# Kernel tuning notes

Measured on AMD Instinct MI355X. Metric: run time of the kernel, lower is better.

The kernel has to match this reference:

```python
import jax, jax.numpy as jnp
import numpy as np

B, T, H = 8, 2048, 1024
THRESHOLD = 0.9
MAX_HOP = 12
LN_EPS = 1e-5


def setup_inputs() -> dict:
    key = jax.random.key(0)
    ks = jax.random.split(key, 5)
    inputs = jax.random.normal(ks[0], (B, T, H), jnp.float32)
    time_enc = jax.random.normal(ks[1], (1, T, H), jnp.float32)
    pos_enc = jax.random.normal(ks[2], (1, MAX_HOP, H), jnp.float32)
    ln_gamma = jnp.ones((H,), jnp.float32)
    ln_beta = jnp.zeros((H,), jnp.float32)
    w_p = jax.random.normal(ks[3], (H,), jnp.float32) / np.float32(np.sqrt(H))
    b_p = jnp.ones((1,), jnp.float32)  # p.bias.data.fill_(1)
    Wt = jax.random.normal(ks[4], (H, H), jnp.float32) / np.float32(np.sqrt(H))
    bt = jnp.zeros((H,), jnp.float32)
    return dict(inputs=inputs, time_enc=time_enc, pos_enc=pos_enc,
                ln_gamma=ln_gamma, ln_beta=ln_beta, w_p=w_p, b_p=b_p,
                Wt=Wt, bt=bt)


def _act_forward(inputs, time_enc, pos_enc, ln_gamma, ln_beta, w_p, b_p, Wt, bt):
    Bv, Tv, _ = inputs.shape
    base = inputs + time_enc[:, :Tv]  # [B,T,H]

    def step(carry, k):
        hp, rem, n_up, prev = carry
        state = base + pos_enc[:, k][:, None, :]  # [B,T,H]
        # LayerNorm
        mu = state.mean(-1, keepdims=True)
        var = state.var(-1, keepdims=True)
        normed = (state - mu) * jax.lax.rsqrt(var + LN_EPS) * ln_gamma + ln_beta
        # halting probability [B,T]
        p = jax.nn.sigmoid(jnp.einsum('bth,h->bt', normed, w_p) + b_p[0])
        sr = (hp < 1.0).astype(state.dtype)
        acc = hp + p * sr
        nh = (acc > THRESHOLD).astype(state.dtype) * sr
        sr = (acc <= THRESHOLD).astype(state.dtype) * sr
        hp = hp + p * sr
        rem = rem + nh * (1.0 - hp)
        hp = hp + nh * rem
        n_up = n_up + sr + nh
        # state update (transformation_fn modeled as Linear Wt, bt)
        uw = (p * sr + nh * rem)[..., None]  # [B,T,1]
        tstate = jnp.einsum('bth,oh->bto', state, Wt) + bt
        new = tstate * uw + prev * (1.0 - uw)
        return (hp, rem, n_up, new), None

    z = jnp.zeros((Bv, Tv), inputs.dtype)
    init = (z, z, z, jnp.zeros_like(inputs))
    # Fixed MAX_HOP iterations: once all tokens halt, still_running and
    # new_halted are identically zero so further steps are exact no-ops,
    # matching the data-dependent while loop of the original module.
    (hp, rem, n_up, prev), _ = jax.lax.scan(step, init, jnp.arange(MAX_HOP))
    return prev, rem, n_up


def reference(inputs, time_enc, pos_enc, ln_gamma, ln_beta, w_p, b_p, Wt, bt):
    return _act_forward(inputs, time_enc, pos_enc, ln_gamma, ln_beta, w_p, b_p, Wt, bt)
```

## Files before the change

kernel.cpp:

```cpp
#include <hip/hip_runtime.h>


#define Hdim 1024
#define Ntok 16384
#define Tdim 2048
#define KHOP 12

typedef unsigned short u16;
typedef __attribute__((ext_vector_type(8))) short bf16x8;
typedef __attribute__((ext_vector_type(4))) float floatx4;
struct __align__(8) u16x4 { u16 x, y, z, w; };

static __device__ inline u16 f2bf(float f) {
    union { float f; unsigned u; } x; x.f = f;
    unsigned r = x.u + 0x7FFFu + ((x.u >> 16) & 1u);
    return (u16)(r >> 16);
}

__global__ __launch_bounds__(256)
void ptwt_kernel(const float* __restrict__ pos,
                 const float* __restrict__ gamma,
                 const float* __restrict__ beta,
                 const float* __restrict__ wp,
                 const float* __restrict__ Wt,
                 float* __restrict__ kst,
                 float* __restrict__ gwArr,
                 float* __restrict__ PT,
                 u16* __restrict__ WtBF) {
    if (blockIdx.x < 13) {
        int lane = threadIdx.x;
        if (lane >= 64) return;
        int b = blockIdx.x;
        if (b == 12) {
            float gw = 0.f, bw = 0.f;
#pragma unroll
            for (int i = 0; i < 16; i++) {
                int h = lane + 64 * i;
                float g = gamma[h] * wp[h];
                gwArr[h] = g;
                gw += g;
                bw += beta[h] * wp[h];
            }
            for (int off = 32; off > 0; off >>= 1) {
                gw += __shfl_xor(gw, off);
                bw += __shfl_xor(bw, off);
            }
            if (lane == 0) { kst[36] = gw; kst[37] = bw; }
        } else {
            int k = b;
            float gw = 0.f;
#pragma unroll
            for (int i = 0; i < 16; i++) {
                int h = lane + 64 * i;
                gw += gamma[h] * wp[h];
            }
            for (int off = 32; off > 0; off >>= 1) gw += __shfl_xor(gw, off);
            float s = 0.f, ss = 0.f, pg = 0.f;
#pragma unroll
            for (int i = 0; i < 16; i++) {
                int h = lane + 64 * i;
                float v = pos[k * Hdim + h];
                s += v; ss += v * v; pg += v * gamma[h] * wp[h];
            }
            for (int off = 32; off > 0; off >>= 1) {
                s += __shfl_xor(s, off);
                ss += __shfl_xor(ss, off);
                pg += __shfl_xor(pg, off);
            }
            if (lane == 0) {
                float mu = s * (1.0f / Hdim);
                kst[k] = mu;
                kst[12 + k] = ss - (float)Hdim * mu * mu;
                kst[24 + k] = pg - mu * gw;
            }
        }
        return;
    }

    __shared__ float red[4][KHOP];
    int o = blockIdx.x - 13;
    int t = threadIdx.x, wave = t >> 6, lane = t & 63;

    float4 w = ((const float4*)(Wt + (size_t)o * Hdim))[t];
    u16x4 ob; ob.x = f2bf(w.x); ob.y = f2bf(w.y); ob.z = f2bf(w.z); ob.w = f2bf(w.w);
    ((u16x4*)(WtBF + (size_t)o * Hdim))[t] = ob;

    const float4* pos4 = (const float4*)pos;
    float acc[KHOP];
#pragma unroll
    for (int k = 0; k < KHOP; k++) {
        float4 p = pos4[k * 256 + t];
        acc[k] = w.x * p.x + w.y * p.y + w.z * p.z + w.w * p.w;
    }
#pragma unroll
    for (int k = 0; k < KHOP; k++)
        for (int off = 32; off > 0; off >>= 1) acc[k] += __shfl_xor(acc[k], off);
    if (lane == 0) {
#pragma unroll
        for (int k = 0; k < KHOP; k++) red[wave][k] = acc[k];
    }
    __syncthreads();
    if (t < KHOP)
        PT[t * Hdim + o] = red[0][t] + red[1][t] + red[2][t] + red[3][t];
}

__global__ __launch_bounds__(512)
void token_kernel(const float* __restrict__ inp, const float* __restrict__ tenc,
                  const float* __restrict__ pos, const float* __restrict__ gwArr,
                  const float* __restrict__ bp, const float* __restrict__ kst,
                  float* __restrict__ SS, float* __restrict__ WW,
                  float* __restrict__ tail, u16* __restrict__ baseBF) {
    __shared__ float sPos[KHOP * Hdim];
    int t = threadIdx.x;
    for (int i = t; i < KHOP * Hdim; i += 512) sPos[i] = pos[i];
    __syncthreads();

    int wave = t >> 6, lane = t & 63;
    int grp = lane >> 4, s = lane & 15;
    int n = blockIdx.x * 32 + wave * 4 + grp;

    const float4* ip4 = (const float4*)(inp + (size_t)n * Hdim);
    const float4* tp4 = (const float4*)(tenc + (size_t)(n & (Tdim - 1)) * Hdim);
    u16x4* ob4 = (u16x4*)(baseBF + (size_t)n * Hdim);
    const float4* gw4 = (const float4*)gwArr;

    float sm = 0.f, ss = 0.f, d1 = 0.f;
    float dk[KHOP];
#pragma unroll
    for (int k = 0; k < KHOP; k++) dk[k] = 0.f;

#pragma unroll
    for (int i = 0; i < 16; i++) {
        int idx = s + 16 * i;
        float4 a = ip4[idx], b = tp4[idx];
        float4 v = make_float4(a.x + b.x, a.y + b.y, a.z + b.z, a.w + b.w);
        u16x4 o; o.x = f2bf(v.x); o.y = f2bf(v.y); o.z = f2bf(v.z); o.w = f2bf(v.w);
        ob4[idx] = o;
        sm += v.x + v.y + v.z + v.w;
        ss += v.x * v.x + v.y * v.y + v.z * v.z + v.w * v.w;
        float4 g = gw4[idx];
        d1 += v.x * g.x + v.y * g.y + v.z * g.z + v.w * g.w;
        int h = idx * 4;
#pragma unroll
        for (int k = 0; k < KHOP; k++) {
            float4 p = *(const float4*)&sPos[k * Hdim + h];
            dk[k] += v.x * p.x + v.y * p.y + v.z * p.z + v.w * p.w;
        }
    }
#pragma unroll
    for (int off = 8; off > 0; off >>= 1) {
        sm += __shfl_xor(sm, off);
        ss += __shfl_xor(ss, off);
        d1 += __shfl_xor(d1, off);
#pragma unroll
        for (int k = 0; k < KHOP; k++) dk[k] += __shfl_xor(dk[k], off);
    }

    if (s == 0) {
        float gwv = kst[36], bwv = kst[37], bpv = bp[0];
        float mu = sm * (1.0f / Hdim);
        float ssb = ss - (float)Hdim * mu * mu;
        float hp = 0.f, rem = 0.f, nu = 0.f;
        float uw[KHOP];
#pragma unroll
        for (int k = 0; k < KHOP; k++) {
            float mup = kst[k], sspk = kst[12 + k], ek = kst[24 + k];
            float ck = dk[k] - (float)Hdim * mu * mup;
            float var = (ssb + sspk + 2.0f * ck) * (1.0f / Hdim);
            float inv = 1.0f / sqrtf(var + 1e-5f);
            float logit = inv * (d1 - mu * gwv + ek) + bwv + bpv;
            float p = 1.0f / (1.0f + expf(-logit));
            float sr = (hp < 1.0f) ? 1.0f : 0.0f;
            float acc = hp + p * sr;
            float nh = (acc > 0.9f) ? sr : 0.0f;
            float sr2 = (acc <= 0.9f) ? sr : 0.0f;
            hp += p * sr2;
            rem += nh * (1.0f - hp);
            hp += nh * rem;
            nu += sr2 + nh;
            uw[k] = p * sr2 + nh * rem;
        }
        float prod = 1.f, S = 0.f;
        float w[KHOP];
#pragma unroll
        for (int k = KHOP - 1; k >= 0; k--) {
            w[k] = uw[k] * prod;
            prod *= (1.0f - uw[k]);
            S += w[k];
        }
        SS[n] = S;
#pragma unroll
        for (int k = 0; k < KHOP; k++) WW[k * Ntok + n] = w[k];
        tail[n] = rem;
        tail[Ntok + n] = nu;
    }
}

__global__ __launch_bounds__(512, 2)
void gemm_bf16(const u16* __restrict__ A, const u16* __restrict__ Bt,
               const float* __restrict__ bt, const float* __restrict__ PT,
               const float* __restrict__ SS, const float* __restrict__ WW,
               float* __restrict__ out) {
    extern __shared__ u16 lds[];
    const int tid = threadIdx.x;
    const int bm = blockIdx.x;
    const int bn = blockIdx.y;
    const int gm = bm * 256, gn = bn * 256;

    const int sr = tid >> 3;
    const int gchunk = ((tid & 7) ^ (sr & 7)) << 3;
    const u16* aStage = A + (size_t)(gm + sr) * Hdim + gchunk;
    const u16* bStage = Bt + (size_t)(gn + sr) * Hdim + gchunk;
    char* ldsA = (char*)lds + (size_t)tid * 16;
    char* ldsB = (char*)lds + 65536 + (size_t)tid * 16;

#define STAGE_TILE(kt_)                                                          \
    do {                                                                         \
        const int s_ = (kt_) & 1;                                                \
        const u16* ap_ = aStage + (kt_) * 64;                                    \
        const u16* bp_ = bStage + (kt_) * 64;                                    \
        char* la_ = ldsA + s_ * 32768;                                           \
        char* lb_ = ldsB + s_ * 32768;                                           \
        _Pragma("unroll")                                                        \
        for (int i_ = 0; i_ < 4; i_++) {                                         \
            __builtin_amdgcn_global_load_lds(                                    \
                (const __attribute__((address_space(1))) void*)(ap_ + (size_t)i_ * 64 * Hdim), \
                (__attribute__((address_space(3))) void*)(la_ + i_ * 8192), 16, 0, 0); \
            __builtin_amdgcn_global_load_lds(                                    \
                (const __attribute__((address_space(1))) void*)(bp_ + (size_t)i_ * 64 * Hdim), \
                (__attribute__((address_space(3))) void*)(lb_ + i_ * 8192), 16, 0, 0); \
        }                                                                        \
    } while (0)

    STAGE_TILE(0);
    STAGE_TILE(1);

    const int wave = tid >> 6, lane = tid & 63;
    const int wr = wave >> 2, wc = wave & 3;
    const int quad = lane >> 4, l16 = lane & 15;
    const int xorl = l16 & 7;
    const int pos0 = ((quad ^ xorl) << 3);
    const int pos1 = (((4 + quad) ^ xorl) << 3);
    const u16* aRd = lds + (size_t)(128 * wr + l16) * 64;
    const u16* bRd = lds + 32768 + (size_t)(64 * wc + l16) * 64;

    floatx4 acc[8][4];
#pragma unroll
    for (int i = 0; i < 8; i++)
#pragma unroll
        for (int j = 0; j < 4; j++) acc[i][j] = (floatx4)0.f;

#pragma unroll 2
    for (int kt = 0; kt < 16; kt++) {
        const int s = kt & 1;
        if (kt < 15) { asm volatile("s_waitcnt vmcnt(8)" ::: "memory"); }
        else         { asm volatile("s_waitcnt vmcnt(0)" ::: "memory"); }
        asm volatile("s_barrier" ::: "memory");

        const u16* aS = aRd + s * 16384;
        const u16* bS = bRd + s * 16384;
        bf16x8 a[4][2], b[4][2];
#pragma unroll
        for (int ni = 0; ni < 4; ni++) {
            b[ni][0] = *(const bf16x8*)&bS[ni * 1024 + pos0];
            b[ni][1] = *(const bf16x8*)&bS[ni * 1024 + pos1];
        }
#pragma unroll
        for (int mi = 0; mi < 4; mi++) {
            a[mi][0] = *(const bf16x8*)&aS[mi * 1024 + pos0];
            a[mi][1] = *(const bf16x8*)&aS[mi * 1024 + pos1];
        }
        __builtin_amdgcn_s_setprio(1);
#pragma unroll
        for (int kk = 0; kk < 2; kk++)
#pragma unroll
            for (int mi = 0; mi < 4; mi++)
#pragma unroll
                for (int ni = 0; ni < 4; ni++)
                    acc[mi][ni] = __builtin_amdgcn_mfma_f32_16x16x32_bf16(
                        a[mi][kk], b[ni][kk], acc[mi][ni], 0, 0, 0);
        __builtin_amdgcn_s_setprio(0);

#pragma unroll
        for (int mi = 0; mi < 4; mi++) {
            a[mi][0] = *(const bf16x8*)&aS[4096 + mi * 1024 + pos0];
            a[mi][1] = *(const bf16x8*)&aS[4096 + mi * 1024 + pos1];
        }
        asm volatile("s_barrier" ::: "memory");
        if (kt < 14) STAGE_TILE(kt + 2);
        __builtin_amdgcn_s_setprio(1);
#pragma unroll
        for (int kk = 0; kk < 2; kk++)
#pragma unroll
            for (int mi = 0; mi < 4; mi++)
#pragma unroll
                for (int ni = 0; ni < 4; ni++)
                    acc[4 + mi][ni] = __builtin_amdgcn_mfma_f32_16x16x32_bf16(
                        a[mi][kk], b[ni][kk], acc[4 + mi][ni], 0, 0, 0);
        __builtin_amdgcn_s_setprio(0);
    }
#undef STAGE_TILE

    const int colBase = gn + 64 * wc;
    float btc[4], PTc[KHOP][4];
#pragma unroll
    for (int ni = 0; ni < 4; ni++) {
        int col = colBase + 16 * ni + l16;
        btc[ni] = bt[col];
#pragma unroll
        for (int k = 0; k < KHOP; k++) PTc[k][ni] = PT[k * Hdim + col];
    }
    const int rowBase = gm + 128 * wr;
#pragma unroll
    for (int mi = 0; mi < 8; mi++) {
        int r0 = rowBase + 16 * mi + quad * 4;
        float Sr[4], Wr[KHOP][4];
#pragma unroll
        for (int reg = 0; reg < 4; reg++) Sr[reg] = SS[r0 + reg];
#pragma unroll
        for (int k = 0; k < KHOP; k++)
#pragma unroll
            for (int reg = 0; reg < 4; reg++) Wr[k][reg] = WW[k * Ntok + r0 + reg];
#pragma unroll
        for (int ni = 0; ni < 4; ni++) {
            int col = colBase + 16 * ni + l16;
#pragma unroll
            for (int reg = 0; reg < 4; reg++) {
                float v = Sr[reg] * (acc[mi][ni][reg] + btc[ni]);
#pragma unroll
                for (int k = 0; k < KHOP; k++) v += Wr[k][reg] * PTc[k][ni];
                out[(size_t)(r0 + reg) * Hdim + col] = v;
            }
        }
    }
}

extern "C" void kernel_launch(void* const* d_in, const int* in_sizes, int n_in,
                              void* d_out, int out_size, void* d_ws, size_t ws_size,
                              hipStream_t stream) {
    const float* inp   = (const float*)d_in[0];
    const float* tenc  = (const float*)d_in[1];
    const float* pos   = (const float*)d_in[2];
    const float* gamma = (const float*)d_in[3];
    const float* beta  = (const float*)d_in[4];
    const float* wp    = (const float*)d_in[5];
    const float* bp    = (const float*)d_in[6];
    const float* Wt    = (const float*)d_in[7];
    const float* bt    = (const float*)d_in[8];
    float* out = (float*)d_out;

    float* W = (float*)d_ws;
    float* kst = W;
    float* gwArr = W + 64;
    float* PT  = gwArr + Hdim;
    float* SS  = PT + KHOP * Hdim;
    float* WW  = SS + Ntok;
    u16* WtBF  = (u16*)(WW + KHOP * Ntok);
    u16* baseBF = WtBF + (size_t)Hdim * Hdim;

    static bool attr_done = false;
    if (!attr_done) {
        (void)hipFuncSetAttribute((const void*)gemm_bf16,
                                  hipFuncAttributeMaxDynamicSharedMemorySize,
                                  131072);
        attr_done = true;
    }

    ptwt_kernel<<<1037, 256, 0, stream>>>(pos, gamma, beta, wp, Wt,
                                          kst, gwArr, PT, WtBF);
    token_kernel<<<512, 512, 0, stream>>>(inp, tenc, pos, gwArr, bp, kst,
                                          SS, WW, out + (size_t)Ntok * Hdim, baseBF);
    gemm_bf16<<<dim3(64, 4), 512, 131072, stream>>>(baseBF, WtBF, bt, PT, SS, WW, out);
}
```

Baseline: 193.2 us.

## Deepen GEMM pipeline to 4-stage BK=32 ring and prefetch token loads

The bf16 GEMM's K loop changes from 16 double-buffered BK=64 tiles with two barriers per step to 32 BK=32 tiles in a four-slot LDS ring, keeping three tiles in flight with a single barrier per step and a new XOR swizzle. The token kernel now software-prefetches its input and time-encoding loads two iterations ahead and declares an occupancy hint of 4 blocks per CU. The aim is to hide global-load latency better and cut barrier count, at the cost of smaller MFMA batches per barrier and possible register pressure in the token kernel.

```diff
diff --git a/kernel.cpp b/kernel.cpp
--- a/kernel.cpp
+++ b/kernel.cpp
@@ -104,7 +104,7 @@
         PT[t * Hdim + o] = red[0][t] + red[1][t] + red[2][t] + red[3][t];
 }
 
-__global__ __launch_bounds__(512)
+__global__ __launch_bounds__(512, 4)
 void token_kernel(const float* __restrict__ inp, const float* __restrict__ tenc,
                   const float* __restrict__ pos, const float* __restrict__ gwArr,
                   const float* __restrict__ bp, const float* __restrict__ kst,
@@ -129,10 +129,15 @@
 #pragma unroll
     for (int k = 0; k < KHOP; k++) dk[k] = 0.f;
 
+    float4 pa0 = ip4[s],      pb0 = tp4[s];
+    float4 pa1 = ip4[s + 16], pb1 = tp4[s + 16];
+
 #pragma unroll
     for (int i = 0; i < 16; i++) {
         int idx = s + 16 * i;
-        float4 a = ip4[idx], b = tp4[idx];
+        float4 a = pa0, b = pb0;
+        pa0 = pa1; pb0 = pb1;
+        if (i < 14) { pa1 = ip4[idx + 32]; pb1 = tp4[idx + 32]; }
         float4 v = make_float4(a.x + b.x, a.y + b.y, a.z + b.z, a.w + b.w);
         u16x4 o; o.x = f2bf(v.x); o.y = f2bf(v.y); o.z = f2bf(v.z); o.w = f2bf(v.w);
         ob4[idx] = o;
@@ -207,42 +212,37 @@
     const int bn = blockIdx.y;
     const int gm = bm * 256, gn = bn * 256;
 
-    const int sr = tid >> 3;
-    const int gchunk = ((tid & 7) ^ (sr & 7)) << 3;
-    const u16* aStage = A + (size_t)(gm + sr) * Hdim + gchunk;
-    const u16* bStage = Bt + (size_t)(gn + sr) * Hdim + gchunk;
-    char* ldsA = (char*)lds + (size_t)tid * 16;
-    char* ldsB = (char*)lds + 65536 + (size_t)tid * 16;
+    const int gch = (((tid & 3) ^ ((tid >> 3) & 3)) << 3);
+    const u16* aStage = A + (size_t)(gm + (tid >> 2)) * Hdim + gch;
+    const u16* bStage = Bt + (size_t)(gn + (tid >> 2)) * Hdim + gch;
+    char* ldsW = (char*)lds + (size_t)tid * 16;
+
+#define GLDS(src_, dstoff_)                                                      \
+    __builtin_amdgcn_global_load_lds(                                            \
+        (const __attribute__((address_space(1))) void*)(src_),                   \
+        (__attribute__((address_space(3))) void*)(ldsW + (dstoff_)), 16, 0, 0)
 
 #define STAGE_TILE(kt_)                                                          \
     do {                                                                         \
-        const int s_ = (kt_) & 1;                                                \
-        const u16* ap_ = aStage + (kt_) * 64;                                    \
-        const u16* bp_ = bStage + (kt_) * 64;                                    \
-        char* la_ = ldsA + s_ * 32768;                                           \
-        char* lb_ = ldsB + s_ * 32768;                                           \
-        _Pragma("unroll")                                                        \
-        for (int i_ = 0; i_ < 4; i_++) {                                         \
-            __builtin_amdgcn_global_load_lds(                                    \
-                (const __attribute__((address_space(1))) void*)(ap_ + (size_t)i_ * 64 * Hdim), \
-                (__attribute__((address_space(3))) void*)(la_ + i_ * 8192), 16, 0, 0); \
-            __builtin_amdgcn_global_load_lds(                                    \
-                (const __attribute__((address_space(1))) void*)(bp_ + (size_t)i_ * 64 * Hdim), \
-                (__attribute__((address_space(3))) void*)(lb_ + i_ * 8192), 16, 0, 0); \
-        }                                                                        \
+        const int so_ = ((kt_) & 3) * 32768;                                     \
+        const u16* ap_ = aStage + (kt_) * 32;                                    \
+        const u16* bp_ = bStage + (kt_) * 32;                                    \
+        GLDS(ap_,                 so_);                     \
+        GLDS(ap_ + 128 * Hdim,    so_ + 8192);              \
+        GLDS(bp_,                 so_ + 16384);             \
+        GLDS(bp_ + 128 * Hdim,    so_ + 24576);             \
     } while (0)
 
     STAGE_TILE(0);
     STAGE_TILE(1);
+    STAGE_TILE(2);
 
     const int wave = tid >> 6, lane = tid & 63;
     const int wr = wave >> 2, wc = wave & 3;
     const int quad = lane >> 4, l16 = lane & 15;
-    const int xorl = l16 & 7;
-    const int pos0 = ((quad ^ xorl) << 3);
-    const int pos1 = (((4 + quad) ^ xorl) << 3);
-    const u16* aRd = lds + (size_t)(128 * wr + l16) * 64;
-    const u16* bRd = lds + 32768 + (size_t)(64 * wc + l16) * 64;
+    const int pos = ((quad ^ ((l16 >> 1) & 3)) << 3);
+    const u16* aRd = lds + (size_t)(128 * wr + l16) * 32 + pos;
+    const u16* bRd = lds + 8192 + (size_t)(64 * wc + l16) * 32 + pos;
 
     floatx4 acc[8][4];
 #pragma unroll
@@ -250,56 +250,35 @@
 #pragma unroll
         for (int j = 0; j < 4; j++) acc[i][j] = (floatx4)0.f;
 
-#pragma unroll 2
-    for (int kt = 0; kt < 16; kt++) {
-        const int s = kt & 1;
-        if (kt < 15) { asm volatile("s_waitcnt vmcnt(8)" ::: "memory"); }
-        else         { asm volatile("s_waitcnt vmcnt(0)" ::: "memory"); }
+#pragma unroll 4
+    for (int kt = 0; kt < 32; kt++) {
+        if (kt <= 29)      { asm volatile("s_waitcnt vmcnt(8)" ::: "memory"); }
+        else if (kt == 30) { asm volatile("s_waitcnt vmcnt(4)" ::: "memory"); }
+        else               { asm volatile("s_waitcnt vmcnt(0)" ::: "memory"); }
         asm volatile("s_barrier" ::: "memory");
 
-        const u16* aS = aRd + s * 16384;
-        const u16* bS = bRd + s * 16384;
-        bf16x8 a[4][2], b[4][2];
-#pragma unroll
-        for (int ni = 0; ni < 4; ni++) {
-            b[ni][0] = *(const bf16x8*)&bS[ni * 1024 + pos0];
-            b[ni][1] = *(const bf16x8*)&bS[ni * 1024 + pos1];
-        }
-#pragma unroll
-        for (int mi = 0; mi < 4; mi++) {
-            a[mi][0] = *(const bf16x8*)&aS[mi * 1024 + pos0];
-            a[mi][1] = *(const bf16x8*)&aS[mi * 1024 + pos1];
-        }
+        if (kt <= 28) STAGE_TILE(kt + 3);
+
+        const int so = (kt & 3) * 16384;
+        const u16* aS = aRd + so;
+        const u16* bS = bRd + so;
+        bf16x8 a[8], b[4];
+#pragma unroll
+        for (int ni = 0; ni < 4; ni++) b[ni] = *(const bf16x8*)&bS[ni * 512];
+#pragma unroll
+        for (int mi = 0; mi < 8; mi++) a[mi] = *(const bf16x8*)&aS[mi * 512];
+
         __builtin_amdgcn_s_setprio(1);
 #pragma unroll
-        for (int kk = 0; kk < 2; kk++)
-#pragma unroll
-            for (int mi = 0; mi < 4; mi++)
-#pragma unroll
-                for (int ni = 0; ni < 4; ni++)
-                    acc[mi][ni] = __builtin_amdgcn_mfma_f32_16x16x32_bf16(
-                        a[mi][kk], b[ni][kk], acc[mi][ni], 0, 0, 0);
+        for (int mi = 0; mi < 8; mi++)
+#pragma unroll
+            for (int ni = 0; ni < 4; ni++)
+                acc[mi][ni] = __builtin_amdgcn_mfma_f32_16x16x32_bf16(
+                    a[mi], b[ni], acc[mi][ni], 0, 0, 0);
         __builtin_amdgcn_s_setprio(0);
-
-#pragma unroll
-        for (int mi = 0; mi < 4; mi++) {
-            a[mi][0] = *(const bf16x8*)&aS[4096 + mi * 1024 + pos0];
-            a[mi][1] = *(const bf16x8*)&aS[4096 + mi * 1024 + pos1];
-        }
-        asm volatile("s_barrier" ::: "memory");
-        if (kt < 14) STAGE_TILE(kt + 2);
-        __builtin_amdgcn_s_setprio(1);
-#pragma unroll
-        for (int kk = 0; kk < 2; kk++)
-#pragma unroll
-            for (int mi = 0; mi < 4; mi++)
-#pragma unroll
-                for (int ni = 0; ni < 4; ni++)
-                    acc[4 + mi][ni] = __builtin_amdgcn_mfma_f32_16x16x32_bf16(
-                        a[mi][kk], b[ni][kk], acc[4 + mi][ni], 0, 0, 0);
-        __builtin_amdgcn_s_setprio(0);
     }
 #undef STAGE_TILE
+#undef GLDS
 
     const int colBase = gn + 64 * wc;
     float btc[4], PTc[KHOP][4];
```

Result: slower. 223.6 us (+15.8%).

## Use 4-wave GEMM blocks with 128x128 warp tiles and prefetch token loads

Applied to the files above, without the earlier changes.

The GEMM block drops from 8 waves to 4, and each wave now computes a 128x128 sub-tile (8x8 MFMA accumulators) instead of 128x64. This raises register-level reuse of the A and B fragments and halves LDS reads per MFMA. Staging is redistributed so each thread issues twice as many global-to-LDS loads, and the wait counts are adjusted to match. The token kernel also gets software-prefetched input loads and an occupancy hint. The larger accumulator array (256 floats per lane) risks high VGPR pressure or spills, and fewer waves per CU means less latency hiding.

```diff
diff --git a/kernel.cpp b/kernel.cpp
--- a/kernel.cpp
+++ b/kernel.cpp
@@ -104,7 +104,7 @@
         PT[t * Hdim + o] = red[0][t] + red[1][t] + red[2][t] + red[3][t];
 }
 
-__global__ __launch_bounds__(512)
+__global__ __launch_bounds__(512, 4)
 void token_kernel(const float* __restrict__ inp, const float* __restrict__ tenc,
                   const float* __restrict__ pos, const float* __restrict__ gwArr,
                   const float* __restrict__ bp, const float* __restrict__ kst,
@@ -129,10 +129,15 @@
 #pragma unroll
     for (int k = 0; k < KHOP; k++) dk[k] = 0.f;
 
+    float4 pa0 = ip4[s],      pb0 = tp4[s];
+    float4 pa1 = ip4[s + 16], pb1 = tp4[s + 16];
+
 #pragma unroll
     for (int i = 0; i < 16; i++) {
         int idx = s + 16 * i;
-        float4 a = ip4[idx], b = tp4[idx];
+        float4 a = pa0, b = pb0;
+        pa0 = pa1; pb0 = pb1;
+        if (i < 14) { pa1 = ip4[idx + 32]; pb1 = tp4[idx + 32]; }
         float4 v = make_float4(a.x + b.x, a.y + b.y, a.z + b.z, a.w + b.w);
         u16x4 o; o.x = f2bf(v.x); o.y = f2bf(v.y); o.z = f2bf(v.z); o.w = f2bf(v.w);
         ob4[idx] = o;
@@ -196,7 +201,7 @@
     }
 }
 
-__global__ __launch_bounds__(512, 2)
+__global__ __launch_bounds__(256, 1)
 void gemm_bf16(const u16* __restrict__ A, const u16* __restrict__ Bt,
                const float* __restrict__ bt, const float* __restrict__ PT,
                const float* __restrict__ SS, const float* __restrict__ WW,
@@ -214,6 +219,11 @@
     char* ldsA = (char*)lds + (size_t)tid * 16;
     char* ldsB = (char*)lds + 65536 + (size_t)tid * 16;
 
+#define GLDS(src_, dst_)                                                         \
+    __builtin_amdgcn_global_load_lds(                                            \
+        (const __attribute__((address_space(1))) void*)(src_),                   \
+        (__attribute__((address_space(3))) void*)(dst_), 16, 0, 0)
+
 #define STAGE_TILE(kt_)                                                          \
     do {                                                                         \
         const int s_ = (kt_) & 1;                                                \
@@ -222,13 +232,9 @@
         char* la_ = ldsA + s_ * 32768;                                           \
         char* lb_ = ldsB + s_ * 32768;                                           \
         _Pragma("unroll")                                                        \
-        for (int i_ = 0; i_ < 4; i_++) {                                         \
-            __builtin_amdgcn_global_load_lds(                                    \
-                (const __attribute__((address_space(1))) void*)(ap_ + (size_t)i_ * 64 * Hdim), \
-                (__attribute__((address_space(3))) void*)(la_ + i_ * 8192), 16, 0, 0); \
-            __builtin_amdgcn_global_load_lds(                                    \
-                (const __attribute__((address_space(1))) void*)(bp_ + (size_t)i_ * 64 * Hdim), \
-                (__attribute__((address_space(3))) void*)(lb_ + i_ * 8192), 16, 0, 0); \
+        for (int i_ = 0; i_ < 8; i_++) {                                         \
+            GLDS(ap_ + (size_t)i_ * 32 * Hdim, la_ + i_ * 4096);                 \
+            GLDS(bp_ + (size_t)i_ * 32 * Hdim, lb_ + i_ * 4096);                 \
         }                                                                        \
     } while (0)
 
@@ -236,75 +242,64 @@
     STAGE_TILE(1);
 
     const int wave = tid >> 6, lane = tid & 63;
-    const int wr = wave >> 2, wc = wave & 3;
+    const int wr = wave >> 1, wc = wave & 1;
     const int quad = lane >> 4, l16 = lane & 15;
     const int xorl = l16 & 7;
     const int pos0 = ((quad ^ xorl) << 3);
     const int pos1 = (((4 + quad) ^ xorl) << 3);
     const u16* aRd = lds + (size_t)(128 * wr + l16) * 64;
-    const u16* bRd = lds + 32768 + (size_t)(64 * wc + l16) * 64;
-
-    floatx4 acc[8][4];
+    const u16* bRd = lds + 32768 + (size_t)(128 * wc + l16) * 64;
+
+    floatx4 acc[8][8];
 #pragma unroll
     for (int i = 0; i < 8; i++)
 #pragma unroll
-        for (int j = 0; j < 4; j++) acc[i][j] = (floatx4)0.f;
-
-#pragma unroll 2
+        for (int j = 0; j < 8; j++) acc[i][j] = (floatx4)0.f;
+
     for (int kt = 0; kt < 16; kt++) {
         const int s = kt & 1;
-        if (kt < 15) { asm volatile("s_waitcnt vmcnt(8)" ::: "memory"); }
+        if (kt < 15) { asm volatile("s_waitcnt vmcnt(16)" ::: "memory"); }
         else         { asm volatile("s_waitcnt vmcnt(0)" ::: "memory"); }
         asm volatile("s_barrier" ::: "memory");
 
         const u16* aS = aRd + s * 16384;
         const u16* bS = bRd + s * 16384;
-        bf16x8 a[4][2], b[4][2];
-#pragma unroll
-        for (int ni = 0; ni < 4; ni++) {
-            b[ni][0] = *(const bf16x8*)&bS[ni * 1024 + pos0];
-            b[ni][1] = *(const bf16x8*)&bS[ni * 1024 + pos1];
-        }
-#pragma unroll
-        for (int mi = 0; mi < 4; mi++) {
-            a[mi][0] = *(const bf16x8*)&aS[mi * 1024 + pos0];
-            a[mi][1] = *(const bf16x8*)&aS[mi * 1024 + pos1];
-        }
+        bf16x8 a0[8], b0[8], a1[8], b1[8];
+#pragma unroll
+        for (int ni = 0; ni < 8; ni++) b0[ni] = *(const bf16x8*)&bS[ni * 1024 + pos0];
+#pragma unroll
+        for (int mi = 0; mi < 8; mi++) a0[mi] = *(const bf16x8*)&aS[mi * 1024 + pos0];
         __builtin_amdgcn_s_setprio(1);
 #pragma unroll
-        for (int kk = 0; kk < 2; kk++)
-#pragma unroll
-            for (int mi = 0; mi < 4; mi++)
-#pragma unroll
-                for (int ni = 0; ni < 4; ni++)
-                    acc[mi][ni] = __builtin_amdgcn_mfma_f32_16x16x32_bf16(
-                        a[mi][kk], b[ni][kk], acc[mi][ni], 0, 0, 0);
+        for (int mi = 0; mi < 8; mi++)
+#pragma unroll
+            for (int ni = 0; ni < 8; ni++)
+                acc[mi][ni] = __builtin_amdgcn_mfma_f32_16x16x32_bf16(
+                    a0[mi], b0[ni], acc[mi][ni], 0, 0, 0);
         __builtin_amdgcn_s_setprio(0);
 
 #pragma unroll
-        for (int mi = 0; mi < 4; mi++) {
-            a[mi][0] = *(const bf16x8*)&aS[4096 + mi * 1024 + pos0];
-            a[mi][1] = *(const bf16x8*)&aS[4096 + mi * 1024 + pos1];
-        }
+        for (int ni = 0; ni < 8; ni++) b1[ni] = *(const bf16x8*)&bS[ni * 1024 + pos1];
+#pragma unroll
+        for (int mi = 0; mi < 8; mi++) a1[mi] = *(const bf16x8*)&aS[mi * 1024 + pos1];
         asm volatile("s_barrier" ::: "memory");
         if (kt < 14) STAGE_TILE(kt + 2);
         __builtin_amdgcn_s_setprio(1);
 #pragma unroll
-        for (int kk = 0; kk < 2; kk++)
-#pragma unroll
-            for (int mi = 0; mi < 4; mi++)
-#pragma unroll
-                for (int ni = 0; ni < 4; ni++)
-                    acc[4 + mi][ni] = __builtin_amdgcn_mfma_f32_16x16x32_bf16(
-                        a[mi][kk], b[ni][kk], acc[4 + mi][ni], 0, 0, 0);
+        for (int mi = 0; mi < 8; mi++)
+#pragma unroll
+            for (int ni = 0; ni < 8; ni++)
+                acc[mi][ni] = __builtin_amdgcn_mfma_f32_16x16x32_bf16(
+                    a1[mi], b1[ni], acc[mi][ni], 0, 0, 0);
         __builtin_amdgcn_s_setprio(0);
     }
 #undef STAGE_TILE
-
-    const int colBase = gn + 64 * wc;
-    float btc[4], PTc[KHOP][4];
-#pragma unroll
-    for (int ni = 0; ni < 4; ni++) {
+#undef GLDS
+
+    const int colBase = gn + 128 * wc;
+    float btc[8], PTc[KHOP][8];
+#pragma unroll
+    for (int ni = 0; ni < 8; ni++) {
         int col = colBase + 16 * ni + l16;
         btc[ni] = bt[col];
 #pragma unroll
@@ -322,7 +317,7 @@
 #pragma unroll
             for (int reg = 0; reg < 4; reg++) Wr[k][reg] = WW[k * Ntok + r0 + reg];
 #pragma unroll
-        for (int ni = 0; ni < 4; ni++) {
+        for (int ni = 0; ni < 8; ni++) {
             int col = colBase + 16 * ni + l16;
 #pragma unroll
             for (int reg = 0; reg < 4; reg++) {
@@ -370,5 +365,5 @@
                                           kst, gwArr, PT, WtBF);
     token_kernel<<<512, 512, 0, stream>>>(inp, tenc, pos, gwArr, bp, kst,
                                           SS, WW, out + (size_t)Ntok * Hdim, baseBF);
-    gemm_bf16<<<dim3(64, 4), 512, 131072, stream>>>(baseBF, WtBF, bt, PT, SS, WW, out);
-}
+    gemm_bf16<<<dim3(64, 4), 256, 131072, stream>>>(baseBF, WtBF, bt, PT, SS, WW, out);
+}
```

Result: no change. 197.0 us (+2.0%).
